# Performance work log

Measured on AMD Instinct MI355X. Metric: run time of the kernel, lower is better.

The kernel has to match this reference:

```python
import jax, jax.numpy as jnp
import numpy as np

N = 100000   # nodes
E = 1600000  # edges (before self loops)
F = 64       # num_features
H = 64       # hidden_channels
C = 10       # num_classes
G = 128      # graphs in batch
NEG_SLOPE = 0.2


def setup_inputs() -> dict:
    key = jax.random.key(0)
    ks = jax.random.split(key, 16)
    x = jax.random.normal(ks[0], (N, F), dtype=jnp.float32)
    edge_index = jax.random.randint(ks[1], (2, E), 0, N, dtype=jnp.int64)
    batch = jnp.sort(jax.random.randint(ks[2], (N,), 0, G, dtype=jnp.int64))
    def glorot(k, shape):
        fan = shape[0] + shape[-1]
        return jax.random.uniform(k, shape, jnp.float32, -1.0, 1.0) * np.sqrt(6.0 / fan)
    return {
        "x": x, "edge_index": edge_index, "batch": batch,
        # GATConv 1 (F -> H)
        "W1": glorot(ks[3], (F, H)), "as1": glorot(ks[4], (H,)), "ad1": glorot(ks[5], (H,)), "b1": jnp.zeros((H,), jnp.float32),
        # GATConv 2 (H -> H)
        "W2": glorot(ks[6], (H, H)), "as2": glorot(ks[7], (H,)), "ad2": glorot(ks[8], (H,)), "b2": jnp.zeros((H,), jnp.float32),
        # MLP head
        "mw1": glorot(ks[9], (H, H)), "mb1": jnp.zeros((H,), jnp.float32),
        "mw2": glorot(ks[10], (H, C)), "mb2": jnp.zeros((C,), jnp.float32),
    }


def gat_conv(x, src, dst, W, a_s, a_d, b):
    # x: [N, Fin] -> h: [N, Fout]
    h = x @ W
    # per-node attention halves, gathered per edge (heads=1)
    al_s = h @ a_s   # [N]
    al_d = h @ a_d   # [N]
    e = jax.nn.leaky_relu(al_s[src] + al_d[dst], NEG_SLOPE)  # [E']
    # segment softmax over incoming edges of each destination node
    m = jax.ops.segment_max(e, dst, num_segments=N)
    ex = jnp.exp(e - m[dst])
    denom = jax.ops.segment_sum(ex, dst, num_segments=N)
    alpha = ex / denom[dst]                                   # [E']
    # weighted scatter-add of source features
    out = jax.ops.segment_sum(alpha[:, None] * h[src], dst, num_segments=N)
    return out + b


def reference(x, edge_index, batch, W1, as1, ad1, b1, W2, as2, ad2, b2, mw1, mb1, mw2, mb2):
    # add self loops (PyG GATConv default)
    loop = jnp.arange(N, dtype=edge_index.dtype)
    src = jnp.concatenate([edge_index[0], loop])
    dst = jnp.concatenate([edge_index[1], loop])

    h = gat_conv(x, src, dst, W1, as1, ad1, b1)
    h = jax.nn.elu(h)  # dropout p=0.5 is identity in eval mode
    h = gat_conv(h, src, dst, W2, as2, ad2, b2)
    h = jax.nn.elu(h)

    h = jax.nn.relu(h @ mw1 + mb1) @ mw2 + mb2   # MLP [N, C]
    return jax.ops.segment_sum(h, batch, num_segments=G)  # global_add_pool [G, C]
```

## Files before the change

### kernel.cpp

```cpp
#include <hip/hip_runtime.h>
#include <hip/hip_bf16.h>
#include <math.h>

#define SHIFT 20.0f
#define T_PER 32
#define TILE (256 * T_PER)
#define BCAP 5248
#define LS_T 1024

typedef __bf16 bf16x8 __attribute__((ext_vector_type(8)));
typedef float  f32x4  __attribute__((ext_vector_type(4)));

__device__ __forceinline__ unsigned f2bf(float f) {
    unsigned u = __float_as_uint(f);
    return (u + 0x7fffu + ((u >> 16) & 1u)) >> 16;
}

__global__ void setup_kernel(int* __restrict__ bcur, int K2,
                             float* __restrict__ Pz, int nPz,
                             const float* __restrict__ W1,
                             const float* __restrict__ as1, const float* __restrict__ ad1,
                             const float* __restrict__ W2,
                             const float* __restrict__ as2, const float* __restrict__ ad2,
                             const float* __restrict__ mw1,
                             uint4* __restrict__ Wf1, uint4* __restrict__ Wf2,
                             uint4* __restrict__ mwf)
{
    int t = threadIdx.x;
    if (blockIdx.x == 0) {
        for (int i = t; i < K2; i += 256) bcur[i * 16] = i * BCAP;
        for (int i = t; i < nPz; i += 256) Pz[i] = 0.f;
        return;
    }
    __shared__ float wasad[256];
    {
        int k = t & 63;
        const float* W  = (t < 128) ? W1 : W2;
        const float* av = (t < 64) ? as1 : (t < 128) ? ad1 : (t < 192) ? as2 : ad2;
        float s = 0.f;
        for (int n = 0; n < 64; n++) s = fmaf(W[k * 64 + n], av[n], s);
        wasad[t] = s;
    }
    __syncthreads();

    for (int idx = t; idx < 1792; idx += 256) {
        const float* W; const float* wv; uint4* dst; int rem;
        if (idx < 640)       { rem = idx;        W = W1;  wv = &wasad[0];   dst = Wf1; }
        else if (idx < 1280) { rem = idx - 640;  W = W2;  wv = &wasad[128]; dst = Wf2; }
        else                 { rem = idx - 1280; W = mw1; wv = nullptr;     dst = mwf; }
        int pair = rem >> 6, l = rem & 63;
        int tt = pair >> 1, s = pair & 1;
        int kb = s * 32 + (l >> 4) * 8;
        unsigned d[4];
        if (tt < 4) {
            int n = tt * 16 + (l & 15);
            #pragma unroll
            for (int j = 0; j < 4; j++)
                d[j] = f2bf(W[(kb + 2 * j) * 64 + n]) |
                       (f2bf(W[(kb + 2 * j + 1) * 64 + n]) << 16);
        } else {
            int n0 = l & 15;
            #pragma unroll
            for (int j = 0; j < 4; j++) {
                float v0 = (n0 == 0) ? wv[kb + 2 * j]     : (n0 == 1) ? wv[64 + kb + 2 * j]     : 0.f;
                float v1 = (n0 == 0) ? wv[kb + 2 * j + 1] : (n0 == 1) ? wv[64 + kb + 2 * j + 1] : 0.f;
                d[j] = f2bf(v0) | (f2bf(v1) << 16);
            }
        }
        dst[pair * 64 + l] = make_uint4(d[0], d[1], d[2], d[3]);
    }
}

__device__ __forceinline__ void multisplit_body(
    unsigned char* ldsraw, const int* __restrict__ esrc, const int* __restrict__ edst,
    int* __restrict__ bcur, unsigned* __restrict__ pairbuf,
    int nE, int tot, int K2, int tile)
{
    int* lhist = (int*)ldsraw;
    int* cur   = lhist + 512;
    int t = threadIdx.x;
    int base = tile * TILE;
    for (int i = t; i < K2; i += 256) lhist[i] = 0;
    __syncthreads();

    #pragma unroll
    for (int i = 0; i < T_PER; i++) {
        int e = base + t + i * 256;
        if (e < tot) {
            int d = (e < nE) ? edst[e] : (e - nE);
            atomicAdd(&lhist[d >> 8], 1);
        }
    }
    __syncthreads();
    for (int i = t; i < K2; i += 256) {
        int c = lhist[i];
        cur[i] = (c > 0) ? atomicAdd(&bcur[i * 16], c) : 0;
    }
    __syncthreads();
    #pragma unroll
    for (int i = 0; i < T_PER; i++) {
        int e = base + t + i * 256;
        if (e < tot) {
            int s = (e < nE) ? esrc[e] : (e - nE);
            int d = (e < nE) ? edst[e] : (e - nE);
            int pos = atomicAdd(&cur[d >> 8], 1);
            pairbuf[pos] = ((unsigned)s << 8) | (unsigned)(d & 255);
        }
    }
}

__device__ __forceinline__ void gemm_body(
    unsigned char* lds, const void* __restrict__ Xv, int x_is_bf16,
    const uint4* __restrict__ Wf, __hip_bfloat16* __restrict__ Hout,
    float* __restrict__ als, float* __restrict__ ald, int nN, int b0)
{
    int t = threadIdx.x, lane = t & 63, wv = t >> 6;

    uint4 wf[10];
    #pragma unroll
    for (int p = 0; p < 10; p++) wf[p] = Wf[p * 64 + lane];

    if (x_is_bf16) {
        const uint4* X4 = (const uint4*)Xv;
        int limit = nN * 8;
        #pragma unroll
        for (int k = 0; k < 8; k++) {
            int dst = t + k * 256;
            int idx = b0 * 8 + dst;
            if (idx < limit) {
                int r = dst >> 3, c = dst & 7;
                *(uint4*)(lds + r * 144 + c * 16) = X4[idx];
            }
        }
    } else {
        const float4* Xf = (const float4*)Xv;
        int limit = nN * 16;
        #pragma unroll
        for (int k = 0; k < 16; k++) {
            int dst = t + k * 256;
            int idx = b0 * 16 + dst;
            if (idx < limit) {
                float4 v = Xf[idx];
                uint2 r2;
                r2.x = f2bf(v.x) | (f2bf(v.y) << 16);
                r2.y = f2bf(v.z) | (f2bf(v.w) << 16);
                int r = dst >> 4, c = dst & 15;
                *(uint2*)(lds + r * 144 + c * 8) = r2;
            }
        }
    }
    __syncthreads();

    f32x4 acc[4][5] = {};
    int rbase = wv * 64;
    #pragma unroll
    for (int s = 0; s < 2; s++) {
        #pragma unroll
        for (int rf = 0; rf < 4; rf++) {
            const uint4 av = *(const uint4*)(lds + (rbase + rf * 16 + (lane & 15)) * 144
                                                 + s * 64 + (lane >> 4) * 16);
            bf16x8 a = __builtin_bit_cast(bf16x8, av);
            #pragma unroll
            for (int tt = 0; tt < 5; tt++) {
                bf16x8 b = __builtin_bit_cast(bf16x8, wf[tt * 2 + s]);
                acc[rf][tt] = __builtin_amdgcn_mfma_f32_16x16x32_bf16(a, b, acc[rf][tt], 0, 0, 0);
            }
        }
    }

    int q = lane >> 4, c = lane & 15;
    #pragma unroll
    for (int rf = 0; rf < 4; rf++) {
        #pragma unroll
        for (int r = 0; r < 4; r++) {
            int n = b0 + rbase + rf * 16 + q * 4 + r;
            if (n < nN) {
                #pragma unroll
                for (int tt = 0; tt < 4; tt++)
                    Hout[(size_t)n * 64 + tt * 16 + c] = __float2bfloat16(acc[rf][tt][r]);
                if (c == 0)      als[n] = acc[rf][4][r];
                else if (c == 1) ald[n] = acc[rf][4][r];
            }
        }
    }
}

__global__ __launch_bounds__(256) void ms_gemm_kernel(
    const int* __restrict__ esrc, const int* __restrict__ edst,
    int* __restrict__ bcur, unsigned* __restrict__ pairbuf,
    int nE, int nN, int K2, int nTiles,
    const void* __restrict__ Xv, const uint4* __restrict__ Wf,
    __hip_bfloat16* __restrict__ Hout,
    float* __restrict__ als, float* __restrict__ ald)
{
    __shared__ __align__(16) unsigned char lds[256 * 144];
    if (blockIdx.x < nTiles) {
        multisplit_body(lds, esrc, edst, bcur, pairbuf, nE, nE + nN, K2, blockIdx.x);
    } else {
        gemm_body(lds, Xv, 0, Wf, Hout, als, ald, nN, (blockIdx.x - nTiles) * 256);
    }
}

__global__ __launch_bounds__(256) void gemm_att_mfma(
    const void* __restrict__ Xv, int x_is_bf16,
    const uint4* __restrict__ Wf,
    __hip_bfloat16* __restrict__ Hout,
    float* __restrict__ als, float* __restrict__ ald, int nN)
{
    __shared__ __align__(16) unsigned char lds[256 * 144];
    gemm_body(lds, Xv, x_is_bf16, Wf, Hout, als, ald, nN, blockIdx.x * 256);
}

__global__ __launch_bounds__(LS_T) void local_scatter_kernel(
    const unsigned* __restrict__ pairbuf, const int* __restrict__ bcur,
    int2* __restrict__ rp2, int* __restrict__ csr_src, int nN, int K2)
{
    __shared__ unsigned seg[BCAP];
    __shared__ int lh[256];
    __shared__ int cur[256];
    __shared__ int psum[256];
    int b = blockIdx.x;
    int t = threadIdx.x;
    int d0 = b * 256;
    int nd = min(256, nN - d0);
    int lo = b * BCAP;
    int hi = bcur[b * 16];
    int len = min(hi - lo, BCAP);

    if (t < 256) lh[t] = 0;
    for (int j = t; j < len; j += LS_T) seg[j] = pairbuf[lo + j];
    __syncthreads();
    for (int j = t; j < len; j += LS_T) atomicAdd(&lh[seg[j] & 255u], 1);
    __syncthreads();

    int v = (t < 256) ? lh[t] : 0;
    if (t < 256) psum[t] = v;
    __syncthreads();
    for (int off = 1; off < 256; off <<= 1) {
        int u = (t < 256 && t >= off) ? psum[t - off] : 0;
        __syncthreads();
        if (t < 256) psum[t] += u;
        __syncthreads();
    }
    if (t < 256) {
        int e0 = lo + psum[t] - v;
        cur[t] = e0;
        if (t < nd) rp2[d0 + t] = make_int2(e0, v);
    }
    __syncthreads();

    for (int j = t; j < len; j += LS_T) {
        unsigned w = seg[j];
        int pos = atomicAdd(&cur[w & 255u], 1);
        csr_src[pos] = (int)(w >> 8);
    }
}

__global__ __launch_bounds__(256) void pull_kernel(
    const int* __restrict__ csr_src, const int2* __restrict__ rp2,
    const unsigned* __restrict__ Hu,
    const float* __restrict__ als, const float* __restrict__ ald,
    const float* __restrict__ bias,
    __hip_bfloat162* __restrict__ out2, int nN)
{
    int lane = threadIdx.x & 63;
    int half = lane >> 5;
    int fl = lane & 31;
    int wid  = (blockIdx.x * blockDim.x + threadIdx.x) >> 6;
    int nw   = (gridDim.x * blockDim.x) >> 6;
    float2 bl2 = ((const float2*)bias)[fl];

    for (int d = wid; d < nN; d += nw) {
        int2 rp = rp2[d];
        int s0 = rp.x, m = rp.y;
        float aldd = ald[d];
        float aclo = 0.f, achi = 0.f, den = 0.f;

        for (int base = 0; base < m; base += 64) {
            int j = base + lane;
            bool v = (j < m);
            int sl = v ? csr_src[s0 + j] : 0;
            float ex = 0.f;
            if (v) {
                float sc = als[sl] + aldd;
                sc = (sc > 0.f) ? sc : 0.2f * sc;
                ex = __expf(sc - SHIFT);
            }
            float es = ex;
            #pragma unroll
            for (int off = 32; off > 0; off >>= 1) es += __shfl_xor(es, off);
            den += es;

            int mm = min(64, m - base);
            int sA = __shfl(sl, half), sB = __shfl(sl, 2 + half);
            float eA = __shfl(ex, half), eB = __shfl(ex, 2 + half);
            unsigned dA = Hu[((unsigned)sA << 5) | fl];
            unsigned dB = Hu[((unsigned)sB << 5) | fl];
            for (int i2 = 0; i2 < mm; i2 += 4) {
                int i4 = (i2 + 4) & 63;
                int   sA2 = __shfl(sl, i4 + half);
                int   sB2 = __shfl(sl, i4 + 2 + half);
                float eA2 = __shfl(ex, i4 + half);
                float eB2 = __shfl(ex, i4 + 2 + half);
                unsigned dA2 = Hu[((unsigned)sA2 << 5) | fl];
                unsigned dB2 = Hu[((unsigned)sB2 << 5) | fl];
                aclo = fmaf(eA, __uint_as_float(dA << 16), aclo);
                achi = fmaf(eA, __uint_as_float(dA & 0xffff0000u), achi);
                aclo = fmaf(eB, __uint_as_float(dB << 16), aclo);
                achi = fmaf(eB, __uint_as_float(dB & 0xffff0000u), achi);
                sA = sA2; sB = sB2; eA = eA2; eB = eB2; dA = dA2; dB = dB2;
            }
        }
        aclo += __shfl_xor(aclo, 32);
        achi += __shfl_xor(achi, 32);
        float v0 = aclo / den + bl2.x;
        float v1 = achi / den + bl2.y;
        v0 = (v0 > 0.f) ? v0 : expm1f(v0);
        v1 = (v1 > 0.f) ? v1 : expm1f(v1);
        if (half == 0) {
            __hip_bfloat162 pk;
            pk.x = __float2bfloat16(v0);
            pk.y = __float2bfloat16(v1);
            out2[((unsigned)d << 5) | fl] = pk;
        }
    }
}

__global__ __launch_bounds__(256) void mlp_pool_mfma(
    const uint4* __restrict__ Hin,
    const uint4* __restrict__ mwf, const float* __restrict__ mb1,
    const int* __restrict__ batch,
    float* __restrict__ P, float* __restrict__ Pcnt, int nN)
{
    __shared__ __align__(16) unsigned char lds[256 * 144];
    int t = threadIdx.x, lane = t & 63, wv = t >> 6;
    int b0 = blockIdx.x * 256;

    uint4 wf[8];
    #pragma unroll
    for (int p = 0; p < 8; p++) wf[p] = mwf[p * 64 + lane];

    int limit = nN * 8;
    #pragma unroll
    for (int k = 0; k < 8; k++) {
        int dst = t + k * 256;
        int idx = b0 * 8 + dst;
        if (idx < limit) {
            int r = dst >> 3, c = dst & 7;
            *(uint4*)(lds + r * 144 + c * 16) = Hin[idx];
        }
    }
    __syncthreads();

    f32x4 acc[4][4] = {};
    int rbase = wv * 64;
    #pragma unroll
    for (int s = 0; s < 2; s++) {
        #pragma unroll
        for (int rf = 0; rf < 4; rf++) {
            const uint4 av = *(const uint4*)(lds + (rbase + rf * 16 + (lane & 15)) * 144
                                                 + s * 64 + (lane >> 4) * 16);
            bf16x8 a = __builtin_bit_cast(bf16x8, av);
            #pragma unroll
            for (int tt = 0; tt < 4; tt++) {
                bf16x8 b = __builtin_bit_cast(bf16x8, wf[tt * 2 + s]);
                acc[rf][tt] = __builtin_amdgcn_mfma_f32_16x16x32_bf16(a, b, acc[rf][tt], 0, 0, 0);
            }
        }
    }

    int q = lane >> 4, c = lane & 15;
    float bl0 = mb1[c], bl1 = mb1[16 + c], bl2 = mb1[32 + c], bl3 = mb1[48 + c];
    float r0 = 0.f, r1 = 0.f, r2 = 0.f, r3 = 0.f, ccnt = 0.f;
    int gcur = -1;
    #pragma unroll
    for (int rf = 0; rf < 4; rf++) {
        #pragma unroll
        for (int r = 0; r < 4; r++) {
            int n = b0 + rbase + rf * 16 + q * 4 + r;
            if (n < nN) {
                int g = batch[n];
                if (g != gcur) {
                    if (gcur >= 0) {
                        atomicAdd(&P[(size_t)gcur * 64 + c],      r0);
                        atomicAdd(&P[(size_t)gcur * 64 + 16 + c], r1);
                        atomicAdd(&P[(size_t)gcur * 64 + 32 + c], r2);
                        atomicAdd(&P[(size_t)gcur * 64 + 48 + c], r3);
                        if (c == 0) atomicAdd(&Pcnt[gcur], ccnt);
                    }
                    gcur = g; r0 = r1 = r2 = r3 = 0.f; ccnt = 0.f;
                }
                r0 += fmaxf(acc[rf][0][r] + bl0, 0.f);
                r1 += fmaxf(acc[rf][1][r] + bl1, 0.f);
                r2 += fmaxf(acc[rf][2][r] + bl2, 0.f);
                r3 += fmaxf(acc[rf][3][r] + bl3, 0.f);
                ccnt += 1.f;
            }
        }
    }
    if (gcur >= 0) {
        atomicAdd(&P[(size_t)gcur * 64 + c],      r0);
        atomicAdd(&P[(size_t)gcur * 64 + 16 + c], r1);
        atomicAdd(&P[(size_t)gcur * 64 + 32 + c], r2);
        atomicAdd(&P[(size_t)gcur * 64 + 48 + c], r3);
        if (c == 0) atomicAdd(&Pcnt[gcur], ccnt);
    }
}

__global__ void head_out_kernel(const float* __restrict__ P,
                                const float* __restrict__ Pcnt,
                                const float* __restrict__ mw2,
                                const float* __restrict__ mb2,
                                float* __restrict__ out, int nOut)
{
    int t = blockIdx.x * blockDim.x + threadIdx.x;
    if (t >= nOut) return;
    int g = t / 10, j = t % 10;
    float s = mb2[j] * Pcnt[g];
    const float* pr = P + (size_t)g * 64;
    #pragma unroll
    for (int k = 0; k < 64; k++) s = fmaf(pr[k], mw2[k * 10 + j], s);
    out[t] = s;
}

extern "C" void kernel_launch(void* const* d_in, const int* in_sizes, int n_in,
                              void* d_out, int out_size, void* d_ws, size_t ws_size,
                              hipStream_t stream)
{
    const float* x   = (const float*)d_in[0];
    const int*  eidx = (const int*)d_in[1];
    const int* batch = (const int*)d_in[2];
    const float* W1  = (const float*)d_in[3];
    const float* as1 = (const float*)d_in[4];
    const float* ad1 = (const float*)d_in[5];
    const float* b1  = (const float*)d_in[6];
    const float* W2  = (const float*)d_in[7];
    const float* as2 = (const float*)d_in[8];
    const float* ad2 = (const float*)d_in[9];
    const float* b2  = (const float*)d_in[10];
    const float* mw1 = (const float*)d_in[11];
    const float* mb1 = (const float*)d_in[12];
    const float* mw2 = (const float*)d_in[13];
    const float* mb2 = (const float*)d_in[14];
    float* out = (float*)d_out;

    int nN = in_sizes[0] / 64;
    int nE = in_sizes[1] / 2;
    int tot = nE + nN;
    int K2 = (nN + 255) >> 8;
    int G  = out_size / 10;
    const int* esrc = eidx;
    const int* edst = eidx + nE;

    float* ws = (float*)d_ws;
    size_t NF = (size_t)nN * 64;
    size_t capTot = (size_t)K2 * BCAP;
    float* bufA   = ws;
    float* bufB   = ws + NF;
    float* als    = ws + 2 * NF;
    float* ald    = als + nN;
    int2* rp2     = (int2*)(ald + nN);
    int* csr_src  = (int*)(rp2 + nN);
    int* bcur     = csr_src + capTot;
    float* P      = (float*)(bcur + K2 * 16 + 15);
    float* Pcnt   = P + (size_t)G * 64;
    uintptr_t wb  = ((uintptr_t)(Pcnt + G) + 255) & ~(uintptr_t)255;
    uint4* Wf1    = (uint4*)wb;
    uint4* Wf2    = Wf1 + 640;
    uint4* mwf    = Wf2 + 640;
    unsigned* pairbuf = (unsigned*)bufA;
    __hip_bfloat16* hbf = (__hip_bfloat16*)bufB;

    dim3 blk(256);
    int nTiles = (tot + TILE - 1) / TILE;
    int nT256 = (nN + 255) / 256;

    setup_kernel<<<2, blk, 0, stream>>>(bcur, K2, P, G * 64 + G,
                                        W1, as1, ad1, W2, as2, ad2, mw1,
                                        Wf1, Wf2, mwf);
    ms_gemm_kernel<<<nTiles + nT256, blk, 0, stream>>>(
        esrc, edst, bcur, pairbuf, nE, nN, K2, nTiles,
        x, Wf1, hbf, als, ald);
    local_scatter_kernel<<<K2, dim3(LS_T), 0, stream>>>(pairbuf, bcur, rp2,
                                                        csr_src, nN, K2);

    pull_kernel<<<2048, blk, 0, stream>>>(csr_src, rp2, (const unsigned*)hbf,
                                          als, ald, b1,
                                          (__hip_bfloat162*)bufA, nN);
    gemm_att_mfma<<<nT256, blk, 0, stream>>>(bufA, 1, Wf2, hbf, als, ald, nN);
    pull_kernel<<<2048, blk, 0, stream>>>(csr_src, rp2, (const unsigned*)hbf,
                                          als, ald, b2,
                                          (__hip_bfloat162*)bufA, nN);

    mlp_pool_mfma<<<nT256, blk, 0, stream>>>((const uint4*)bufA, mwf, mb1,
                                             batch, P, Pcnt, nN);
    head_out_kernel<<<(out_size + 255) / 256, blk, 0, stream>>>(P, Pcnt, mw2,
                                                                mb2, out, out_size);
}
```

Baseline: 291.5 us.

## Stage multisplit tile in LDS before coalesced scatter to global bucket buffer

The multisplit phase now computes a block-local exclusive prefix over bucket counts, writes each edge into a locally sorted LDS staging buffer along with its bucket id, and then copies the tile out to global memory so consecutive threads write mostly contiguous addresses. This replaces the previous random per-edge scattered global writes. In exchange it adds a 256-step scan with repeated barriers and raises the LDS allocation of the fused kernel to about 53KB. That larger allocation can lower occupancy for the GEMM blocks that share the same kernel.

```diff
diff --git a/kernel.cpp b/kernel.cpp
--- a/kernel.cpp
+++ b/kernel.cpp
@@ -7,6 +7,7 @@
 #define TILE (256 * T_PER)
 #define BCAP 5248
 #define LS_T 1024
+#define MS_LDS 54272
 
 typedef __bf16 bf16x8 __attribute__((ext_vector_type(8)));
 typedef float  f32x4  __attribute__((ext_vector_type(4)));
@@ -76,11 +77,16 @@
     int* __restrict__ bcur, unsigned* __restrict__ pairbuf,
     int nE, int tot, int K2, int tile)
 {
-    int* lhist = (int*)ldsraw;
-    int* cur   = lhist + 512;
+    int* lcur   = (int*)ldsraw;
+    int* ldelta = lcur + 512;
+    int* psum   = ldelta + 512;
+    unsigned* seg = (unsigned*)(psum + 256);
+    unsigned short* bkt = (unsigned short*)(seg + TILE);
     int t = threadIdx.x;
     int base = tile * TILE;
-    for (int i = t; i < K2; i += 256) lhist[i] = 0;
+    int cnt_tile = min(TILE, tot - base);
+
+    for (int i = t; i < 512; i += 256) lcur[i] = 0;
     __syncthreads();
 
     #pragma unroll
@@ -88,25 +94,47 @@
         int e = base + t + i * 256;
         if (e < tot) {
             int d = (e < nE) ? edst[e] : (e - nE);
-            atomicAdd(&lhist[d >> 8], 1);
-        }
-    }
-    __syncthreads();
-    for (int i = t; i < K2; i += 256) {
-        int c = lhist[i];
-        cur[i] = (c > 0) ? atomicAdd(&bcur[i * 16], c) : 0;
-    }
-    __syncthreads();
+            atomicAdd(&lcur[d >> 8], 1);
+        }
+    }
+    __syncthreads();
+
+    int v0 = lcur[2 * t], v1 = lcur[2 * t + 1];
+    int ps = v0 + v1;
+    psum[t] = ps;
+    __syncthreads();
+    for (int off = 1; off < 256; off <<= 1) {
+        int u = (t >= off) ? psum[t - off] : 0;
+        __syncthreads();
+        psum[t] += u;
+        __syncthreads();
+    }
+    int st0 = psum[t] - ps;
+    int st1 = st0 + v0;
+    lcur[2 * t] = st0;
+    lcur[2 * t + 1] = st1;
+    if (v0 > 0 && 2 * t < K2)
+        ldelta[2 * t]     = atomicAdd(&bcur[(2 * t) * 16],     v0) - st0;
+    if (v1 > 0 && 2 * t + 1 < K2)
+        ldelta[2 * t + 1] = atomicAdd(&bcur[(2 * t + 1) * 16], v1) - st1;
+    __syncthreads();
+
     #pragma unroll
     for (int i = 0; i < T_PER; i++) {
         int e = base + t + i * 256;
         if (e < tot) {
             int s = (e < nE) ? esrc[e] : (e - nE);
             int d = (e < nE) ? edst[e] : (e - nE);
-            int pos = atomicAdd(&cur[d >> 8], 1);
-            pairbuf[pos] = ((unsigned)s << 8) | (unsigned)(d & 255);
-        }
-    }
+            int b = d >> 8;
+            int p = atomicAdd(&lcur[b], 1);
+            seg[p] = ((unsigned)s << 8) | (unsigned)(d & 255);
+            bkt[p] = (unsigned short)b;
+        }
+    }
+    __syncthreads();
+
+    for (int j = t; j < cnt_tile; j += 256)
+        pairbuf[j + ldelta[bkt[j]]] = seg[j];
 }
 
 __device__ __forceinline__ void gemm_body(
@@ -193,7 +221,7 @@
     __hip_bfloat16* __restrict__ Hout,
     float* __restrict__ als, float* __restrict__ ald)
 {
-    __shared__ __align__(16) unsigned char lds[256 * 144];
+    __shared__ __align__(16) unsigned char lds[MS_LDS];
     if (blockIdx.x < nTiles) {
         multisplit_body(lds, esrc, edst, bcur, pairbuf, nE, nE + nN, K2, blockIdx.x);
     } else {
```

Result: no change. 290.5 us (-0.3%).
